# Optimization experiments

Measured on AMD Instinct MI355X. Metric: run time of the kernel, lower is better.

## Reference

```python
import jax, jax.numpy as jnp
import numpy as np

N_IN, N_HID, N_OUT = 128, 256, 128
B, T = 64, 2048


def setup_inputs() -> dict:
    key = jax.random.key(0)
    ks = jax.random.split(key, 10)
    s_in = 1.0 / np.sqrt(N_IN)
    s_h = 1.0 / np.sqrt(N_HID)
    return {
        "input_signal": jax.random.normal(ks[0], (B, T, N_IN), dtype=jnp.float32),
        "W_in": jax.random.uniform(ks[1], (N_HID, N_IN), jnp.float32, -s_in, s_in),
        "b_in": jax.random.uniform(ks[2], (N_HID,), jnp.float32, -s_in, s_in),
        "W_ih": jax.random.uniform(ks[3], (N_HID, N_HID), jnp.float32, -s_h, s_h),
        "b_ih": jax.random.uniform(ks[4], (N_HID,), jnp.float32, -s_h, s_h),
        "W_hh": jax.random.uniform(ks[5], (N_HID, N_HID), jnp.float32, -s_h, s_h),
        "b_hh": jax.random.uniform(ks[6], (N_HID,), jnp.float32, -s_h, s_h),
        "W_out": jax.random.uniform(ks[7], (N_OUT, N_HID), jnp.float32, -s_h, s_h),
        "b_out": jax.random.uniform(ks[8], (N_OUT,), jnp.float32, -s_h, s_h),
    }


def reference(input_signal, W_in, b_in, W_ih, b_ih, W_hh, b_hh, W_out, b_out):
    # x_t = relu(in_layer(u_t)); h_t = relu(tanh(W_ih x_t + b_ih + W_hh h_{t-1} + b_hh))
    # out_t = out_layer(h_t)
    x = jax.nn.relu(jnp.einsum('bti,hi->bth', input_signal, W_in) + b_in)
    # Precompute the input-to-hidden projection for all timesteps (batched GEMM),
    # leaving only the sequential h @ W_hh recurrence inside the scan.
    pre = jnp.einsum('bth,gh->tbg', x, W_ih) + b_ih  # [T, B, H]
    h0 = jnp.zeros((input_signal.shape[0], W_hh.shape[0]), dtype=input_signal.dtype)

    def step(h, pre_t):
        h_new = jax.nn.relu(jnp.tanh(pre_t + h @ W_hh.T + b_hh))
        return h_new, h_new

    _, hs = jax.lax.scan(step, h0, pre)            # hs: [T, B, H]
    hidden_list = jnp.transpose(hs, (1, 0, 2))     # [B, T, H]
    output_list = jnp.einsum('bth,oh->bto', hidden_list, W_out) + b_out  # [B, T, O]
    return hidden_list, output_list
```

## Files before the change

kernel.cpp:

```cpp
#include <hip/hip_runtime.h>
#include <hip/hip_fp16.h>

typedef _Float16 f16;
typedef __attribute__((ext_vector_type(2))) _Float16 f16x2;
typedef __attribute__((ext_vector_type(8))) _Float16 f16x8;
typedef __attribute__((ext_vector_type(4))) float f32x4;

constexpr int BATCH = 64;
constexpr int TLEN  = 2048;
constexpr int NIN   = 128;
constexpr int NHID  = 256;
constexpr int NOUT  = 128;
constexpr long MROWS = (long)BATCH * TLEN;
constexpr float CSC = 2.8853900817779268f;

__device__ __forceinline__ float exp2f_hw(float x) {
#if __has_builtin(__builtin_amdgcn_exp2f)
  return __builtin_amdgcn_exp2f(x);
#else
  return __expf(x * 0.6931471805599453f);
#endif
}
__device__ __forceinline__ float rcp_hw(float x) {
#if __has_builtin(__builtin_amdgcn_rcpf)
  return __builtin_amdgcn_rcpf(x);
#else
  return 1.0f / x;
#endif
}
__device__ __forceinline__ float fdot2f(unsigned int a, unsigned int b, float c) {
#if __has_builtin(__builtin_amdgcn_fdot2)
  return __builtin_amdgcn_fdot2(__builtin_bit_cast(f16x2, a),
                                __builtin_bit_cast(f16x2, b), c, false);
#else
  f16x2 av = __builtin_bit_cast(f16x2, a);
  f16x2 bv = __builtin_bit_cast(f16x2, b);
  return c + (float)av.x * (float)bv.x + (float)av.y * (float)bv.y;
#endif
}
template<int CTRL>
__device__ __forceinline__ float dpp_xor(float x) {
  int r = __builtin_amdgcn_update_dpp(0, __builtin_bit_cast(int, x),
                                      CTRL, 0xF, 0xF, true);
  return __builtin_bit_cast(float, r);
}
__device__ __forceinline__ void barrier_lds() {
  asm volatile("s_waitcnt lgkmcnt(0)" ::: "memory");
  __builtin_amdgcn_s_barrier();
  asm volatile("" ::: "memory");
}

__global__ void cvt_weights(const float* __restrict__ Win, const float* __restrict__ Wih,
                            const float* __restrict__ Whh, const float* __restrict__ Wout,
                            f16* __restrict__ dst) {
  int i = blockIdx.x * blockDim.x + threadIdx.x;
  if (i < 32768) {
    float v = Win[i]; f16 h = (f16)v;
    dst[i] = h; dst[32768 + i] = (f16)(v - (float)h);
  } else if (i < 98304) {
    int j = i - 32768; float v = Wih[j]; f16 h = (f16)v;
    dst[65536 + j] = h; dst[131072 + j] = (f16)(v - (float)h);
  } else if (i < 163840) {
    int j = i - 98304; dst[196608 + j] = (f16)(CSC * Whh[j]);
  } else if (i < 196608) {
    int j = i - 163840; dst[262144 + j] = (f16)Wout[j];
  }
}

constexpr int BM = 64, BN = 64, BK = 64;

template<int MODE>
__global__ __launch_bounds__(256)
void gemm_kernel(const void* __restrict__ Ap, const void* __restrict__ Ap2,
                 const f16* __restrict__ Bh_, const f16* __restrict__ Bl_,
                 const float* __restrict__ bias, const float* __restrict__ bias2,
                 void* __restrict__ Cp, void* __restrict__ Cp2,
                 int K, int N) {
  __shared__ __align__(16) f16 Ah[BM][BK + 8];
  __shared__ __align__(16) f16 Al[BM][BK + 8];
  __shared__ __align__(16) f16 Bh[BN][BK + 8];
  __shared__ __align__(16) f16 Bl[BN][BK + 8];

  const int tid  = threadIdx.x;
  const int lane = tid & 63;
  const int wid  = tid >> 6;
  const int wm = wid >> 1, wn = wid & 1;
  const long row0 = (long)blockIdx.x * BM;
  const int  col0 = blockIdx.y * BN;
  const int r  = tid >> 2;
  const int cc = (tid & 3) * 16;

  f32x4 acc[2][2] = {};

  for (int k0 = 0; k0 < K; k0 += BK) {
    if constexpr (MODE == 1) {
      const float* src = (const float*)Ap + (row0 + r) * (long)K + k0 + cc;
      #pragma unroll
      for (int q = 0; q < 4; ++q) {
        float4 v = ((const float4*)src)[q];
        f16 h0 = (f16)v.x, h1 = (f16)v.y, h2 = (f16)v.z, h3 = (f16)v.w;
        Ah[r][cc + 4*q + 0] = h0;  Al[r][cc + 4*q + 0] = (f16)(v.x - (float)h0);
        Ah[r][cc + 4*q + 1] = h1;  Al[r][cc + 4*q + 1] = (f16)(v.y - (float)h1);
        Ah[r][cc + 4*q + 2] = h2;  Al[r][cc + 4*q + 2] = (f16)(v.z - (float)h2);
        Ah[r][cc + 4*q + 3] = h3;  Al[r][cc + 4*q + 3] = (f16)(v.w - (float)h3);
      }
    } else if constexpr (MODE == 2) {
      const f16* sh = (const f16*)Ap  + (row0 + r) * (long)K + k0 + cc;
      const f16* sl = (const f16*)Ap2 + (row0 + r) * (long)K + k0 + cc;
      *(uint4*)&Ah[r][cc]     = *(const uint4*)sh;
      *(uint4*)&Ah[r][cc + 8] = *(const uint4*)(sh + 8);
      *(uint4*)&Al[r][cc]     = *(const uint4*)sl;
      *(uint4*)&Al[r][cc + 8] = *(const uint4*)(sl + 8);
    } else {
      const f16* sh = (const f16*)Ap + (row0 + r) * (long)K + k0 + cc;
      *(uint4*)&Ah[r][cc]     = *(const uint4*)sh;
      *(uint4*)&Ah[r][cc + 8] = *(const uint4*)(sh + 8);
    }
    {
      const f16* sh = Bh_ + (col0 + r) * (long)K + k0 + cc;
      *(uint4*)&Bh[r][cc]     = *(const uint4*)sh;
      *(uint4*)&Bh[r][cc + 8] = *(const uint4*)(sh + 8);
      if constexpr (MODE != 3) {
        const f16* sl = Bl_ + (col0 + r) * (long)K + k0 + cc;
        *(uint4*)&Bl[r][cc]     = *(const uint4*)sl;
        *(uint4*)&Bl[r][cc + 8] = *(const uint4*)(sl + 8);
      }
    }
    __syncthreads();

    #pragma unroll
    for (int ks = 0; ks < BK / 32; ++ks) {
      const int ko = ks * 32 + (lane >> 4) * 8;
      const int ra = wm * 32 + (lane & 15);
      const int rb = wn * 32 + (lane & 15);
      f16x8 a0 = *(const f16x8*)&Ah[ra][ko];
      f16x8 a1 = *(const f16x8*)&Ah[ra + 16][ko];
      f16x8 b0 = *(const f16x8*)&Bh[rb][ko];
      f16x8 b1 = *(const f16x8*)&Bh[rb + 16][ko];
      acc[0][0] = __builtin_amdgcn_mfma_f32_16x16x32_f16(a0, b0, acc[0][0], 0, 0, 0);
      acc[0][1] = __builtin_amdgcn_mfma_f32_16x16x32_f16(a0, b1, acc[0][1], 0, 0, 0);
      acc[1][0] = __builtin_amdgcn_mfma_f32_16x16x32_f16(a1, b0, acc[1][0], 0, 0, 0);
      acc[1][1] = __builtin_amdgcn_mfma_f32_16x16x32_f16(a1, b1, acc[1][1], 0, 0, 0);
      if constexpr (MODE != 3) {
        f16x8 la0 = *(const f16x8*)&Al[ra][ko];
        f16x8 la1 = *(const f16x8*)&Al[ra + 16][ko];
        f16x8 lb0 = *(const f16x8*)&Bl[rb][ko];
        f16x8 lb1 = *(const f16x8*)&Bl[rb + 16][ko];
        acc[0][0] = __builtin_amdgcn_mfma_f32_16x16x32_f16(a0, lb0, acc[0][0], 0, 0, 0);
        acc[0][0] = __builtin_amdgcn_mfma_f32_16x16x32_f16(la0, b0, acc[0][0], 0, 0, 0);
        acc[0][1] = __builtin_amdgcn_mfma_f32_16x16x32_f16(a0, lb1, acc[0][1], 0, 0, 0);
        acc[0][1] = __builtin_amdgcn_mfma_f32_16x16x32_f16(la0, b1, acc[0][1], 0, 0, 0);
        acc[1][0] = __builtin_amdgcn_mfma_f32_16x16x32_f16(a1, lb0, acc[1][0], 0, 0, 0);
        acc[1][0] = __builtin_amdgcn_mfma_f32_16x16x32_f16(la1, b0, acc[1][0], 0, 0, 0);
        acc[1][1] = __builtin_amdgcn_mfma_f32_16x16x32_f16(a1, lb1, acc[1][1], 0, 0, 0);
        acc[1][1] = __builtin_amdgcn_mfma_f32_16x16x32_f16(la1, b1, acc[1][1], 0, 0, 0);
      }
    }
    __syncthreads();
  }

  #pragma unroll
  for (int mi = 0; mi < 2; ++mi)
    #pragma unroll
    for (int ni = 0; ni < 2; ++ni)
      #pragma unroll
      for (int q = 0; q < 4; ++q) {
        long row = row0 + wm * 32 + mi * 16 + (lane >> 4) * 4 + q;
        int  col = col0 + wn * 32 + ni * 16 + (lane & 15);
        if constexpr (MODE == 1) {
          float v = fmaxf(acc[mi][ni][q] + bias[col], 0.0f);
          f16 h = (f16)v;
          ((f16*)Cp )[row * (long)N + col] = h;
          ((f16*)Cp2)[row * (long)N + col] = (f16)(v - (float)h);
        } else if constexpr (MODE == 2) {
          float v = (acc[mi][ni][q] + bias[col] + bias2[col]) * CSC;
          ((float*)Cp)[row * (long)N + col] = v;
        } else {
          ((float*)Cp)[row * (long)N + col] = acc[mi][ni][q] + bias[col];
        }
      }
}

#define STEP(K, SRC, DST, P) do {                                            \
  unsigned int hs[32];                                                       \
  _Pragma("unroll")                                                          \
  for (int q = 0; q < 8; ++q) {                                              \
    uint4 v = *(const uint4*)((SRC) + roff[q]);                              \
    hs[4*q+0] = v.x; hs[4*q+1] = v.y; hs[4*q+2] = v.z; hs[4*q+3] = v.w;      \
  }                                                                          \
  float a0a = 0.f, a1a = 0.f, a0b = 0.f, a1b = 0.f;                          \
  _Pragma("unroll")                                                          \
  for (int kk = 0; kk < 16; ++kk) {                                          \
    a0a = fdot2f(wr0[kk], hs[kk], a0a);                                      \
    a1a = fdot2f(wr1[kk], hs[kk], a1a);                                      \
  }                                                                          \
  _Pragma("unroll")                                                          \
  for (int kk = 16; kk < 32; ++kk) {                                         \
    a0b = fdot2f(wr0[kk], hs[kk], a0b);                                      \
    a1b = fdot2f(wr1[kk], hs[kk], a1b);                                      \
  }                                                                          \
  float a0 = a0a + a0b, a1 = a1a + a1b;                                      \
  float keep = s0 ? a1 : a0;                                                 \
  float send = s0 ? a0 : a1;                                                 \
  float t1 = keep + dpp_xor<0xB1>(send);       \
  float z  = t1 + dpp_xor<0x4E>(t1) + (P);              \
  float ee = exp2f_hw(z);                                                    \
  float hv = fmaxf(fmaf(-2.0f, rcp_hw(ee + 1.0f), 1.0f), 0.0f);              \
  f16 hf = (f16)hv;                                                          \
  if (!s1) *(f16*)((DST) + wo) = hf;              \
  else     hp[(K) * 256] = hf;                  \
} while (0)

__global__ __launch_bounds__(512, 1)
void rec_kernel(const float* __restrict__ pre, const f16* __restrict__ W2,
                f16* __restrict__ h16) {
  const int b    = blockIdx.x;
  const int tid  = threadIdx.x;
  const int lane = tid & 63;
  const int w    = tid >> 6;
  const int jj   = lane & 3;
  const int grp  = (lane >> 2) | (w << 4);
  const int s0   = lane & 1;
  const int s1   = (lane >> 1) & 1;
  const int G    = grp * 2;
  const int g    = G + s0;

  __shared__ __align__(16) char hb[2][512];

  unsigned int wr0[32], wr1[32];
  #pragma unroll
  for (int q = 0; q < 8; ++q) {
    int c = (q + 2 * jj) & 7;
    uint4 v0 = *(const uint4*)(W2 + (size_t)G * 256 + 64 * jj + 8 * c);
    uint4 v1 = *(const uint4*)(W2 + (size_t)(G + 1) * 256 + 64 * jj + 8 * c);
    wr0[4*q+0] = v0.x; wr0[4*q+1] = v0.y; wr0[4*q+2] = v0.z; wr0[4*q+3] = v0.w;
    wr1[4*q+0] = v1.x; wr1[4*q+1] = v1.y; wr1[4*q+2] = v1.z; wr1[4*q+3] = v1.w;
  }
  if (tid < 128) ((unsigned int*)&hb[0][0])[tid] = 0u;
  __syncthreads();

  int roff[8];
  #pragma unroll
  for (int q = 0; q < 8; ++q) roff[q] = 128 * jj + 16 * ((q + 2 * jj) & 7);
  const int wo = 2 * g;

  const float* pp  = pre + (size_t)b * TLEN * 256 + g;
  f16*         hp  = h16 + (size_t)b * TLEN * 256 + g;
  const float* ppf = pp + 1024;

  float p0 = pp[0];
  float p1 = pp[256];
  float p2 = pp[512];
  float p3 = pp[768];

  const char* hb0 = &hb[0][0];
  char*       hb1 = &hb[1][0];

  #pragma unroll 1
  for (int t = 0; t < TLEN; t += 4) {
    float n0 = ppf[0];
    float n1 = ppf[256];
    float n2 = ppf[512];
    float n3 = ppf[768];
    STEP(0, hb0, hb1, p0);
    barrier_lds();
    STEP(1, hb1, (char*)hb0, p1);
    barrier_lds();
    STEP(2, hb0, hb1, p2);
    barrier_lds();
    STEP(3, hb1, (char*)hb0, p3);
    barrier_lds();
    p0 = n0; p1 = n1; p2 = n2; p3 = n3;
    ppf += 1024;
    hp  += 1024;
  }
}

__global__ __launch_bounds__(256)
void cvt_h(const f16* __restrict__ src, float* __restrict__ dst, long n) {
  long i0 = ((long)blockIdx.x * 256 + threadIdx.x) * 8;
  long stride = (long)gridDim.x * 256 * 8;
  for (long i = i0; i < n; i += stride) {
    f16x8 v = *(const f16x8*)(src + i);
    float4 a = {(float)v[0], (float)v[1], (float)v[2], (float)v[3]};
    float4 bq = {(float)v[4], (float)v[5], (float)v[6], (float)v[7]};
    *(float4*)(dst + i) = a;
    *(float4*)(dst + i + 4) = bq;
  }
}

extern "C" void kernel_launch(void* const* d_in, const int* in_sizes, int n_in,
                              void* d_out, int out_size, void* d_ws, size_t ws_size,
                              hipStream_t stream) {
  const float* input = (const float*)d_in[0];
  const float* W_in  = (const float*)d_in[1];
  const float* b_in  = (const float*)d_in[2];
  const float* W_ih  = (const float*)d_in[3];
  const float* b_ih  = (const float*)d_in[4];
  const float* W_hh  = (const float*)d_in[5];
  const float* b_hh  = (const float*)d_in[6];
  const float* W_out = (const float*)d_in[7];
  const float* b_out = (const float*)d_in[8];

  float* hidden = (float*)d_out;
  float* outp   = (float*)d_out + MROWS * NHID;

  char* ws = (char*)d_ws;
  const size_t xh_off  = 0;
  const size_t xl_off  = (size_t)MROWS * NHID * 2;
  const size_t pre_off = xl_off * 2;
  const size_t w_off   = pre_off + (size_t)MROWS * NHID * 4;
  const size_t need    = w_off + 294912ull * 2;
  if (ws_size < need) return;

  f16*   x_hi  = (f16*)(ws + xh_off);
  f16*   x_lo  = (f16*)(ws + xl_off);
  float* pre   = (float*)(ws + pre_off);
  f16*   wbase = (f16*)(ws + w_off);
  f16 *WinH = wbase,           *WinL = wbase + 32768;
  f16 *WihH = wbase + 65536,   *WihL = wbase + 131072;
  f16 *Whh16 = wbase + 196608, *Wout16 = wbase + 262144;
  f16* h16 = x_hi;

  cvt_weights<<<768, 256, 0, stream>>>(W_in, W_ih, W_hh, W_out, wbase);

  dim3 g12((unsigned)(MROWS / BM), NHID / BN);
  gemm_kernel<1><<<g12, 256, 0, stream>>>(input, nullptr, WinH, WinL, b_in, nullptr,
                                          x_hi, x_lo, NIN, NHID);
  gemm_kernel<2><<<g12, 256, 0, stream>>>(x_hi, x_lo, WihH, WihL, b_ih, b_hh,
                                          pre, nullptr, NHID, NHID);

  rec_kernel<<<BATCH, 512, 0, stream>>>(pre, Whh16, h16);

  cvt_h<<<2048, 256, 0, stream>>>(h16, hidden, MROWS * NHID);

  dim3 g3((unsigned)(MROWS / BM), NOUT / BN);
  gemm_kernel<3><<<g3, 256, 0, stream>>>(h16, nullptr, Wout16, nullptr, b_out, nullptr,
                                         outp, nullptr, NHID, NOUT);
}
```

Before: 1.108 ms.

## Run recurrence on MFMA with eight batches per block in time-major layout

The recurrent step moves from per-lane fdot2 dot products, one block per batch, to MFMA 16x16x32 f16 tiles. Each block now handles 8 batch rows (half of the 16 MFMA columns), so the launch shrinks from 64 blocks to 8. The pre-activation GEMM now writes its output time-major so each step's loads are contiguous across batches, and the hidden state goes through swizzled LDS double buffers. The aim is to cut per-step latency of the serial chain with matrix cores, at the cost of using far fewer CUs and leaving half of each MFMA idle.

```diff
diff --git a/kernel.cpp b/kernel.cpp
--- a/kernel.cpp
+++ b/kernel.cpp
@@ -3,6 +3,7 @@
 
 typedef _Float16 f16;
 typedef __attribute__((ext_vector_type(2))) _Float16 f16x2;
+typedef __attribute__((ext_vector_type(4))) _Float16 f16x4;
 typedef __attribute__((ext_vector_type(8))) _Float16 f16x8;
 typedef __attribute__((ext_vector_type(4))) float f32x4;
 
@@ -27,22 +28,6 @@
 #else
   return 1.0f / x;
 #endif
-}
-__device__ __forceinline__ float fdot2f(unsigned int a, unsigned int b, float c) {
-#if __has_builtin(__builtin_amdgcn_fdot2)
-  return __builtin_amdgcn_fdot2(__builtin_bit_cast(f16x2, a),
-                                __builtin_bit_cast(f16x2, b), c, false);
-#else
-  f16x2 av = __builtin_bit_cast(f16x2, a);
-  f16x2 bv = __builtin_bit_cast(f16x2, b);
-  return c + (float)av.x * (float)bv.x + (float)av.y * (float)bv.y;
-#endif
-}
-template<int CTRL>
-__device__ __forceinline__ float dpp_xor(float x) {
-  int r = __builtin_amdgcn_update_dpp(0, __builtin_bit_cast(int, x),
-                                      CTRL, 0xF, 0xF, true);
-  return __builtin_bit_cast(float, r);
 }
 __device__ __forceinline__ void barrier_lds() {
   asm volatile("s_waitcnt lgkmcnt(0)" ::: "memory");
@@ -174,104 +159,125 @@
           ((f16*)Cp2)[row * (long)N + col] = (f16)(v - (float)h);
         } else if constexpr (MODE == 2) {
           float v = (acc[mi][ni][q] + bias[col] + bias2[col]) * CSC;
-          ((float*)Cp)[row * (long)N + col] = v;
+          long prow = (row & (long)(TLEN - 1)) * BATCH + (row >> 11);
+          ((float*)Cp)[prow * (long)N + col] = v;
         } else {
           ((float*)Cp)[row * (long)N + col] = acc[mi][ni][q] + bias[col];
         }
       }
 }
 
-#define STEP(K, SRC, DST, P) do {                                            \
-  unsigned int hs[32];                                                       \
-  _Pragma("unroll")                                                          \
-  for (int q = 0; q < 8; ++q) {                                              \
-    uint4 v = *(const uint4*)((SRC) + roff[q]);                              \
-    hs[4*q+0] = v.x; hs[4*q+1] = v.y; hs[4*q+2] = v.z; hs[4*q+3] = v.w;      \
-  }                                                                          \
-  float a0a = 0.f, a1a = 0.f, a0b = 0.f, a1b = 0.f;                          \
-  _Pragma("unroll")                                                          \
-  for (int kk = 0; kk < 16; ++kk) {                                          \
-    a0a = fdot2f(wr0[kk], hs[kk], a0a);                                      \
-    a1a = fdot2f(wr1[kk], hs[kk], a1a);                                      \
-  }                                                                          \
-  _Pragma("unroll")                                                          \
-  for (int kk = 16; kk < 32; ++kk) {                                         \
-    a0b = fdot2f(wr0[kk], hs[kk], a0b);                                      \
-    a1b = fdot2f(wr1[kk], hs[kk], a1b);                                      \
-  }                                                                          \
-  float a0 = a0a + a0b, a1 = a1a + a1b;                                      \
-  float keep = s0 ? a1 : a0;                                                 \
-  float send = s0 ? a0 : a1;                                                 \
-  float t1 = keep + dpp_xor<0xB1>(send);       \
-  float z  = t1 + dpp_xor<0x4E>(t1) + (P);              \
-  float ee = exp2f_hw(z);                                                    \
-  float hv = fmaxf(fmaf(-2.0f, rcp_hw(ee + 1.0f), 1.0f), 0.0f);              \
-  f16 hf = (f16)hv;                                                          \
-  if (!s1) *(f16*)((DST) + wo) = hf;              \
-  else     hp[(K) * 256] = hf;                  \
+#define RSTEP(S, SO, DO_, P0, P1) do {                                        \
+  if (valid) {                                                                \
+    _Pragma("unroll")                                                         \
+    for (int c = 0; c < 8; ++c)                                               \
+      hB[c] = *(const f16x8*)(hbase + (SO) + roff[c]);                        \
+  }                                                                           \
+  f32x4 aA0 = (P0), aA1 = (P1);                                               \
+  f32x4 aB0 = {0.f, 0.f, 0.f, 0.f};                                           \
+  f32x4 aB1 = {0.f, 0.f, 0.f, 0.f};                                           \
+  _Pragma("unroll")                                                           \
+  for (int c = 0; c < 4; ++c) {                                               \
+    aA0 = __builtin_amdgcn_mfma_f32_16x16x32_f16(wA[0][c],     hB[c],     aA0, 0, 0, 0); \
+    aA1 = __builtin_amdgcn_mfma_f32_16x16x32_f16(wA[1][c],     hB[c],     aA1, 0, 0, 0); \
+    aB0 = __builtin_amdgcn_mfma_f32_16x16x32_f16(wA[0][c + 4], hB[c + 4], aB0, 0, 0, 0); \
+    aB1 = __builtin_amdgcn_mfma_f32_16x16x32_f16(wA[1][c + 4], hB[c + 4], aB1, 0, 0, 0); \
+  }                                                                           \
+  f16x4 h0, h1;                                                               \
+  _Pragma("unroll")                                                           \
+  for (int q = 0; q < 4; ++q) {                                               \
+    float z0 = aA0[q] + aB0[q];                                               \
+    float z1 = aA1[q] + aB1[q];                                               \
+    float e0 = exp2f_hw(z0);                                                  \
+    float e1 = exp2f_hw(z1);                                                  \
+    float v0 = fmaxf(fmaf(-2.0f, rcp_hw(e0 + 1.0f), 1.0f), 0.0f);             \
+    float v1 = fmaxf(fmaf(-2.0f, rcp_hw(e1 + 1.0f), 1.0f), 0.0f);             \
+    h0[q] = (f16)v0;                                                          \
+    h1[q] = (f16)v1;                                                          \
+  }                                                                           \
+  if (valid) {                                                                \
+    *(f16x4*)(hbase + (DO_) + wb0) = h0;              \
+    *(f16x4*)(hbase + (DO_) + wb1) = h1;              \
+    *(f16x4*)(hp + (S) * 256)      = h0;              \
+    *(f16x4*)(hp + (S) * 256 + 16) = h1;              \
+  }                                                                           \
+  barrier_lds();                                                              \
 } while (0)
 
 __global__ __launch_bounds__(512, 1)
-void rec_kernel(const float* __restrict__ pre, const f16* __restrict__ W2,
-                f16* __restrict__ h16) {
-  const int b    = blockIdx.x;
+void rec_mfma(const float* __restrict__ pre, const f16* __restrict__ Whh,
+              f16* __restrict__ h16) {
+  const int blk  = blockIdx.x;
   const int tid  = threadIdx.x;
   const int lane = tid & 63;
   const int w    = tid >> 6;
-  const int jj   = lane & 3;
-  const int grp  = (lane >> 2) | (w << 4);
-  const int s0   = lane & 1;
-  const int s1   = (lane >> 1) & 1;
-  const int G    = grp * 2;
-  const int g    = G + s0;
-
-  __shared__ __align__(16) char hb[2][512];
-
-  unsigned int wr0[32], wr1[32];
+  const int col  = lane & 15;
+  const int kg   = lane >> 4;
+  const bool valid = (col < 8);
+  const int bq   = col & 7;
+  const long bglob = (long)blk * 8 + bq;
+
+  __shared__ __align__(16) char hb[8192];
+  char* hbase = (char*)hb;
+
+  f16x8 wA[2][8];
   #pragma unroll
-  for (int q = 0; q < 8; ++q) {
-    int c = (q + 2 * jj) & 7;
-    uint4 v0 = *(const uint4*)(W2 + (size_t)G * 256 + 64 * jj + 8 * c);
-    uint4 v1 = *(const uint4*)(W2 + (size_t)(G + 1) * 256 + 64 * jj + 8 * c);
-    wr0[4*q+0] = v0.x; wr0[4*q+1] = v0.y; wr0[4*q+2] = v0.z; wr0[4*q+3] = v0.w;
-    wr1[4*q+0] = v1.x; wr1[4*q+1] = v1.y; wr1[4*q+2] = v1.z; wr1[4*q+3] = v1.w;
-  }
-  if (tid < 128) ((unsigned int*)&hb[0][0])[tid] = 0u;
+  for (int t = 0; t < 2; ++t)
+    #pragma unroll
+    for (int c = 0; c < 8; ++c)
+      wA[t][c] = *(const f16x8*)(Whh + (size_t)(32 * w + 16 * t + col) * 256
+                                 + c * 32 + kg * 8);
+
+  {
+    uint4 z = {0u, 0u, 0u, 0u};
+    *(uint4*)(hbase + tid * 16) = z;
+  }
   __syncthreads();
 
+  const int rbase = bq * 512 + ((kg * 16) ^ ((bq & 3) << 4)) + ((bq & 4) << 4);
   int roff[8];
   #pragma unroll
-  for (int q = 0; q < 8; ++q) roff[q] = 128 * jj + 16 * ((q + 2 * jj) & 7);
-  const int wo = 2 * g;
-
-  const float* pp  = pre + (size_t)b * TLEN * 256 + g;
-  f16*         hp  = h16 + (size_t)b * TLEN * 256 + g;
-  const float* ppf = pp + 1024;
-
-  float p0 = pp[0];
-  float p1 = pp[256];
-  float p2 = pp[512];
-  float p3 = pp[768];
-
-  const char* hb0 = &hb[0][0];
-  char*       hb1 = &hb[1][0];
+  for (int c = 0; c < 8; ++c) roff[c] = rbase ^ (c * 64);
+  const int wb0   = bq * 512 + ((8 * kg) ^ ((bq & 1) << 4)) + ((bq & 2) << 4)
+                  + ((64 * w) ^ ((bq & 4) << 4));
+  const int wb1   = wb0 ^ 32;
+
+  const float* pp  = pre + (size_t)bglob * 256 + 32 * w + 4 * kg;
+  f16*         hp  = h16 + (size_t)bglob * TLEN * 256 + 32 * w + 4 * kg;
+  const float* ppf = pp + 4 * 16384;
+
+  f32x4 p00 = *(const f32x4*)(pp);
+  f32x4 p01 = *(const f32x4*)(pp + 16);
+  f32x4 p10 = *(const f32x4*)(pp + 16384);
+  f32x4 p11 = *(const f32x4*)(pp + 16400);
+  f32x4 p20 = *(const f32x4*)(pp + 32768);
+  f32x4 p21 = *(const f32x4*)(pp + 32784);
+  f32x4 p30 = *(const f32x4*)(pp + 49152);
+  f32x4 p31 = *(const f32x4*)(pp + 49168);
+
+  f16x8 hB[8] = {};
 
   #pragma unroll 1
   for (int t = 0; t < TLEN; t += 4) {
-    float n0 = ppf[0];
-    float n1 = ppf[256];
-    float n2 = ppf[512];
-    float n3 = ppf[768];
-    STEP(0, hb0, hb1, p0);
-    barrier_lds();
-    STEP(1, hb1, (char*)hb0, p1);
-    barrier_lds();
-    STEP(2, hb0, hb1, p2);
-    barrier_lds();
-    STEP(3, hb1, (char*)hb0, p3);
-    barrier_lds();
-    p0 = n0; p1 = n1; p2 = n2; p3 = n3;
-    ppf += 1024;
+    f32x4 n00 = {}, n01 = {}, n10 = {}, n11 = {};
+    f32x4 n20 = {}, n21 = {}, n30 = {}, n31 = {};
+    if (t + 4 < TLEN) {
+      n00 = *(const f32x4*)(ppf);
+      n01 = *(const f32x4*)(ppf + 16);
+      n10 = *(const f32x4*)(ppf + 16384);
+      n11 = *(const f32x4*)(ppf + 16400);
+      n20 = *(const f32x4*)(ppf + 32768);
+      n21 = *(const f32x4*)(ppf + 32784);
+      n30 = *(const f32x4*)(ppf + 49152);
+      n31 = *(const f32x4*)(ppf + 49168);
+    }
+    RSTEP(0, 0,    4096, p00, p01);
+    RSTEP(1, 4096, 0,    p10, p11);
+    RSTEP(2, 0,    4096, p20, p21);
+    RSTEP(3, 4096, 0,    p30, p31);
+    p00 = n00; p01 = n01; p10 = n10; p11 = n11;
+    p20 = n20; p21 = n21; p30 = n30; p31 = n31;
+    ppf += 65536;
     hp  += 1024;
   }
 }
@@ -330,7 +336,7 @@
   gemm_kernel<2><<<g12, 256, 0, stream>>>(x_hi, x_lo, WihH, WihL, b_ih, b_hh,
                                           pre, nullptr, NHID, NHID);
 
-  rec_kernel<<<BATCH, 512, 0, stream>>>(pre, Whh16, h16);
+  rec_mfma<<<8, 512, 0, stream>>>(pre, Whh16, h16);
 
   cvt_h<<<2048, 256, 0, stream>>>(h16, hidden, MROWS * NHID);
 
```

Measured after the change: 1.984 ms. +79.0%, slower.

## Split recurrence K-dimension eight ways per output group with cross-half permlane reduction

Applied to the files above, without the earlier changes.

Changes the recurrent matvec work split so each lane covers a 32-wide K slice for 4 hidden outputs (eight lanes per group of four), instead of a 64-wide slice for 2 outputs. Each step now does half as many LDS reads and dot products per lane, at the cost of an extra reduction stage that swaps values between wave halves with permlane32_swap or ds_bpermute. The aim is a shorter per-step critical path in the sequential recurrence. The extra cross-lane hop adds latency, and the LDS and W_hh access patterns are remapped.

```diff
diff --git a/kernel.cpp b/kernel.cpp
--- a/kernel.cpp
+++ b/kernel.cpp
@@ -43,6 +43,18 @@
   int r = __builtin_amdgcn_update_dpp(0, __builtin_bit_cast(int, x),
                                       CTRL, 0xF, 0xF, true);
   return __builtin_bit_cast(float, r);
+}
+__device__ __forceinline__ float xor32_partner(float x, int lane) {
+#if __has_builtin(__builtin_amdgcn_permlane32_swap)
+  auto r = __builtin_amdgcn_permlane32_swap(
+      __builtin_bit_cast(unsigned int, x), __builtin_bit_cast(unsigned int, x),
+      false, false);
+  unsigned int pv = (lane < 32) ? r[1] : r[0];
+  return __builtin_bit_cast(float, pv);
+#else
+  return __builtin_bit_cast(float, __builtin_amdgcn_ds_bpermute(
+      ((lane ^ 32) << 2), __builtin_bit_cast(int, x)));
+#endif
 }
 __device__ __forceinline__ void barrier_lds() {
   asm volatile("s_waitcnt lgkmcnt(0)" ::: "memory");
@@ -182,33 +194,45 @@
 }
 
 #define STEP(K, SRC, DST, P) do {                                            \
-  unsigned int hs[32];                                                       \
+  unsigned int hs[16];                                                       \
   _Pragma("unroll")                                                          \
-  for (int q = 0; q < 8; ++q) {                                              \
+  for (int q = 0; q < 4; ++q) {                                              \
     uint4 v = *(const uint4*)((SRC) + roff[q]);                              \
     hs[4*q+0] = v.x; hs[4*q+1] = v.y; hs[4*q+2] = v.z; hs[4*q+3] = v.w;      \
   }                                                                          \
-  float a0a = 0.f, a1a = 0.f, a0b = 0.f, a1b = 0.f;                          \
+  float sA0 = 0.f, sA1 = 0.f, sA2 = 0.f, sA3 = 0.f;                          \
+  float sB0 = 0.f, sB1 = 0.f, sB2 = 0.f, sB3 = 0.f;                          \
   _Pragma("unroll")                                                          \
-  for (int kk = 0; kk < 16; ++kk) {                                          \
-    a0a = fdot2f(wr0[kk], hs[kk], a0a);                                      \
-    a1a = fdot2f(wr1[kk], hs[kk], a1a);                                      \
+  for (int m = 0; m < 8; ++m) {                                              \
+    sA0 = fdot2f(wr[0][m], hs[m], sA0);                                      \
+    sA1 = fdot2f(wr[1][m], hs[m], sA1);                                      \
+    sA2 = fdot2f(wr[2][m], hs[m], sA2);                                      \
+    sA3 = fdot2f(wr[3][m], hs[m], sA3);                                      \
   }                                                                          \
   _Pragma("unroll")                                                          \
-  for (int kk = 16; kk < 32; ++kk) {                                         \
-    a0b = fdot2f(wr0[kk], hs[kk], a0b);                                      \
-    a1b = fdot2f(wr1[kk], hs[kk], a1b);                                      \
+  for (int m = 8; m < 16; ++m) {                                             \
+    sB0 = fdot2f(wr[0][m], hs[m], sB0);                                      \
+    sB1 = fdot2f(wr[1][m], hs[m], sB1);                                      \
+    sB2 = fdot2f(wr[2][m], hs[m], sB2);                                      \
+    sB3 = fdot2f(wr[3][m], hs[m], sB3);                                      \
   }                                                                          \
-  float a0 = a0a + a0b, a1 = a1a + a1b;                                      \
-  float keep = s0 ? a1 : a0;                                                 \
-  float send = s0 ? a0 : a1;                                                 \
-  float t1 = keep + dpp_xor<0xB1>(send);       \
-  float z  = t1 + dpp_xor<0x4E>(t1) + (P);              \
+  float sv0 = sA0 + sB0, sv1 = sA1 + sB1;                                    \
+  float sv2 = sA2 + sB2, sv3 = sA3 + sB3;                                    \
+                               \
+  float k0 = s0 ? sv1 : sv0, d0 = s0 ? sv0 : sv1;                            \
+  float k1 = s0 ? sv3 : sv2, d1 = s0 ? sv2 : sv3;                            \
+  float t0 = k0 + dpp_xor<0xB1>(d0);                                         \
+  float t1 = k1 + dpp_xor<0xB1>(d1);                                         \
+                              \
+  float rk = s1 ? t1 : t0, rs = s1 ? t0 : t1;                                \
+  float z2 = rk + dpp_xor<0x4E>(rs);                                         \
+                                                \
+  float z  = z2 + xor32_partner(z2, lane) + (P);                             \
   float ee = exp2f_hw(z);                                                    \
   float hv = fmaxf(fmaf(-2.0f, rcp_hw(ee + 1.0f), 1.0f), 0.0f);              \
   f16 hf = (f16)hv;                                                          \
-  if (!s1) *(f16*)((DST) + wo) = hf;              \
-  else     hp[(K) * 256] = hf;                  \
+  if (lane < 32) *(f16*)((DST) + wo) = hf;        \
+  else           hp[(K) * 256] = hf;            \
 } while (0)
 
 __global__ __launch_bounds__(512, 1)
@@ -218,30 +242,29 @@
   const int tid  = threadIdx.x;
   const int lane = tid & 63;
   const int w    = tid >> 6;
-  const int jj   = lane & 3;
-  const int grp  = (lane >> 2) | (w << 4);
+  const int jj   = (lane & 3) | ((lane >> 5) << 2);
   const int s0   = lane & 1;
   const int s1   = (lane >> 1) & 1;
-  const int G    = grp * 2;
-  const int g    = G + s0;
+  const int G8   = ((lane >> 2) & 7) | (w << 3);
+  const int g    = 32 * w + (lane & 31);
 
   __shared__ __align__(16) char hb[2][512];
 
-  unsigned int wr0[32], wr1[32];
+  unsigned int wr[4][16];
   #pragma unroll
-  for (int q = 0; q < 8; ++q) {
-    int c = (q + 2 * jj) & 7;
-    uint4 v0 = *(const uint4*)(W2 + (size_t)G * 256 + 64 * jj + 8 * c);
-    uint4 v1 = *(const uint4*)(W2 + (size_t)(G + 1) * 256 + 64 * jj + 8 * c);
-    wr0[4*q+0] = v0.x; wr0[4*q+1] = v0.y; wr0[4*q+2] = v0.z; wr0[4*q+3] = v0.w;
-    wr1[4*q+0] = v1.x; wr1[4*q+1] = v1.y; wr1[4*q+2] = v1.z; wr1[4*q+3] = v1.w;
-  }
+  for (int i = 0; i < 4; ++i)
+    #pragma unroll
+    for (int q = 0; q < 4; ++q) {
+      int c = (q + jj) & 3;
+      uint4 v = *(const uint4*)(W2 + (size_t)(4 * G8 + i) * 256 + 32 * jj + 8 * c);
+      wr[i][4*q+0] = v.x; wr[i][4*q+1] = v.y; wr[i][4*q+2] = v.z; wr[i][4*q+3] = v.w;
+    }
   if (tid < 128) ((unsigned int*)&hb[0][0])[tid] = 0u;
   __syncthreads();
 
-  int roff[8];
+  int roff[4];
   #pragma unroll
-  for (int q = 0; q < 8; ++q) roff[q] = 128 * jj + 16 * ((q + 2 * jj) & 7);
+  for (int q = 0; q < 4; ++q) roff[q] = 64 * jj + 16 * ((q + jj) & 3);
   const int wo = 2 * g;
 
   const float* pp  = pre + (size_t)b * TLEN * 256 + g;
```

After: 1.194 ms. 7.8% more time.

## Use MFMA 16x16x32 f16 for the recurrent matvec instead of dot2 plus DPP

Applied to the files above, without the earlier changes.

Replaces the per-lane fdot2 dot products and DPP cross-lane reductions in the sequential recurrence with MFMA 16x16x32 f16 instructions. Each wave holds 32 rows of W_hh as MFMA A-operands and broadcasts the hidden state as the B operand. Only one column of the output tile is actually used. Pre-activations are loaded as f32x4 vectors and h is written in f16x4 chunks. This trades wasted MFMA throughput (15 of 16 columns unused) for fewer instructions and no shuffle reductions on the latency-critical per-step path, but MFMA latency may dominate each step.

```diff
diff --git a/kernel.cpp b/kernel.cpp
--- a/kernel.cpp
+++ b/kernel.cpp
@@ -3,6 +3,7 @@
 
 typedef _Float16 f16;
 typedef __attribute__((ext_vector_type(2))) _Float16 f16x2;
+typedef __attribute__((ext_vector_type(4))) _Float16 f16x4;
 typedef __attribute__((ext_vector_type(8))) _Float16 f16x8;
 typedef __attribute__((ext_vector_type(4))) float f32x4;
 
@@ -27,22 +28,6 @@
 #else
   return 1.0f / x;
 #endif
-}
-__device__ __forceinline__ float fdot2f(unsigned int a, unsigned int b, float c) {
-#if __has_builtin(__builtin_amdgcn_fdot2)
-  return __builtin_amdgcn_fdot2(__builtin_bit_cast(f16x2, a),
-                                __builtin_bit_cast(f16x2, b), c, false);
-#else
-  f16x2 av = __builtin_bit_cast(f16x2, a);
-  f16x2 bv = __builtin_bit_cast(f16x2, b);
-  return c + (float)av.x * (float)bv.x + (float)av.y * (float)bv.y;
-#endif
-}
-template<int CTRL>
-__device__ __forceinline__ float dpp_xor(float x) {
-  int r = __builtin_amdgcn_update_dpp(0, __builtin_bit_cast(int, x),
-                                      CTRL, 0xF, 0xF, true);
-  return __builtin_bit_cast(float, r);
 }
 __device__ __forceinline__ void barrier_lds() {
   asm volatile("s_waitcnt lgkmcnt(0)" ::: "memory");
@@ -181,34 +166,39 @@
       }
 }
 
-#define STEP(K, SRC, DST, P) do {                                            \
-  unsigned int hs[32];                                                       \
+#define RSTEP(S, SRC, DST, PA, PB) do {                                      \
+  f16x8 hB[8];                                                               \
   _Pragma("unroll")                                                          \
-  for (int q = 0; q < 8; ++q) {                                              \
-    uint4 v = *(const uint4*)((SRC) + roff[q]);                              \
-    hs[4*q+0] = v.x; hs[4*q+1] = v.y; hs[4*q+2] = v.z; hs[4*q+3] = v.w;      \
+  for (int c = 0; c < 8; ++c)                                                \
+    hB[c] = *(const f16x8*)((SRC) + 64 * c + 16 * kg);                       \
+  f32x4 aA0 = {0.f,0.f,0.f,0.f}, aB0 = {0.f,0.f,0.f,0.f};                    \
+  f32x4 aA1 = {0.f,0.f,0.f,0.f}, aB1 = {0.f,0.f,0.f,0.f};                    \
+  _Pragma("unroll")                                                          \
+  for (int c = 0; c < 4; ++c) {                                              \
+    aA0 = __builtin_amdgcn_mfma_f32_16x16x32_f16(wA[0][c],     hB[c],     aA0, 0, 0, 0); \
+    aA1 = __builtin_amdgcn_mfma_f32_16x16x32_f16(wA[1][c],     hB[c],     aA1, 0, 0, 0); \
+    aB0 = __builtin_amdgcn_mfma_f32_16x16x32_f16(wA[0][c + 4], hB[c + 4], aB0, 0, 0, 0); \
+    aB1 = __builtin_amdgcn_mfma_f32_16x16x32_f16(wA[1][c + 4], hB[c + 4], aB1, 0, 0, 0); \
   }                                                                          \
-  float a0a = 0.f, a1a = 0.f, a0b = 0.f, a1b = 0.f;                          \
+  f16x4 h0, h1;                                                              \
   _Pragma("unroll")                                                          \
-  for (int kk = 0; kk < 16; ++kk) {                                          \
-    a0a = fdot2f(wr0[kk], hs[kk], a0a);                                      \
-    a1a = fdot2f(wr1[kk], hs[kk], a1a);                                      \
+  for (int q = 0; q < 4; ++q) {                                              \
+    float z0 = aA0[q] + aB0[q] + (PA)[q];                                    \
+    float z1 = aA1[q] + aB1[q] + (PB)[q];                                    \
+    float e0 = exp2f_hw(z0);                                                 \
+    float e1 = exp2f_hw(z1);                                                 \
+    float v0 = fmaxf(fmaf(-2.0f, rcp_hw(e0 + 1.0f), 1.0f), 0.0f);            \
+    float v1 = fmaxf(fmaf(-2.0f, rcp_hw(e1 + 1.0f), 1.0f), 0.0f);            \
+    h0[q] = (f16)v0;                                                         \
+    h1[q] = (f16)v1;                                                         \
   }                                                                          \
-  _Pragma("unroll")                                                          \
-  for (int kk = 16; kk < 32; ++kk) {                                         \
-    a0b = fdot2f(wr0[kk], hs[kk], a0b);                                      \
-    a1b = fdot2f(wr1[kk], hs[kk], a1b);                                      \
+  if (col == 0) {                                                            \
+    *(f16x4*)((DST) + wo)      = h0;         \
+    *(f16x4*)((DST) + wo + 32) = h1;         \
+  } else if (col == 1) {                                                     \
+    *(f16x4*)(hp + (S) * 256)      = h0;              \
+    *(f16x4*)(hp + (S) * 256 + 16) = h1;              \
   }                                                                          \
-  float a0 = a0a + a0b, a1 = a1a + a1b;                                      \
-  float keep = s0 ? a1 : a0;                                                 \
-  float send = s0 ? a0 : a1;                                                 \
-  float t1 = keep + dpp_xor<0xB1>(send);       \
-  float z  = t1 + dpp_xor<0x4E>(t1) + (P);              \
-  float ee = exp2f_hw(z);                                                    \
-  float hv = fmaxf(fmaf(-2.0f, rcp_hw(ee + 1.0f), 1.0f), 0.0f);              \
-  f16 hf = (f16)hv;                                                          \
-  if (!s1) *(f16*)((DST) + wo) = hf;              \
-  else     hp[(K) * 256] = hf;                  \
 } while (0)
 
 __global__ __launch_bounds__(512, 1)
@@ -218,59 +208,61 @@
   const int tid  = threadIdx.x;
   const int lane = tid & 63;
   const int w    = tid >> 6;
-  const int jj   = lane & 3;
-  const int grp  = (lane >> 2) | (w << 4);
-  const int s0   = lane & 1;
-  const int s1   = (lane >> 1) & 1;
-  const int G    = grp * 2;
-  const int g    = G + s0;
+  const int col  = lane & 15;
+  const int kg   = lane >> 4;
 
   __shared__ __align__(16) char hb[2][512];
 
-  unsigned int wr0[32], wr1[32];
+  f16x8 wA[2][8];
   #pragma unroll
-  for (int q = 0; q < 8; ++q) {
-    int c = (q + 2 * jj) & 7;
-    uint4 v0 = *(const uint4*)(W2 + (size_t)G * 256 + 64 * jj + 8 * c);
-    uint4 v1 = *(const uint4*)(W2 + (size_t)(G + 1) * 256 + 64 * jj + 8 * c);
-    wr0[4*q+0] = v0.x; wr0[4*q+1] = v0.y; wr0[4*q+2] = v0.z; wr0[4*q+3] = v0.w;
-    wr1[4*q+0] = v1.x; wr1[4*q+1] = v1.y; wr1[4*q+2] = v1.z; wr1[4*q+3] = v1.w;
-  }
-  if (tid < 128) ((unsigned int*)&hb[0][0])[tid] = 0u;
+  for (int t = 0; t < 2; ++t)
+    #pragma unroll
+    for (int c = 0; c < 8; ++c)
+      wA[t][c] = *(const f16x8*)(W2 + (size_t)(32 * w + 16 * t + col) * 256
+                                 + c * 32 + kg * 8);
+
+  if (tid < 256) ((unsigned int*)&hb[0][0])[tid] = 0u;
   __syncthreads();
 
-  int roff[8];
-  #pragma unroll
-  for (int q = 0; q < 8; ++q) roff[q] = 128 * jj + 16 * ((q + 2 * jj) & 7);
-  const int wo = 2 * g;
-
-  const float* pp  = pre + (size_t)b * TLEN * 256 + g;
-  f16*         hp  = h16 + (size_t)b * TLEN * 256 + g;
+  const int wo = 64 * w + 8 * kg;
+  const int g0 = 32 * w + 4 * kg;
+
+  const float* pp  = pre + (size_t)b * TLEN * 256 + g0;
+  f16*         hp  = h16 + (size_t)b * TLEN * 256 + g0;
   const float* ppf = pp + 1024;
 
-  float p0 = pp[0];
-  float p1 = pp[256];
-  float p2 = pp[512];
-  float p3 = pp[768];
+  f32x4 p00 = *(const f32x4*)(pp);
+  f32x4 p01 = *(const f32x4*)(pp + 16);
+  f32x4 p10 = *(const f32x4*)(pp + 256);
+  f32x4 p11 = *(const f32x4*)(pp + 272);
+  f32x4 p20 = *(const f32x4*)(pp + 512);
+  f32x4 p21 = *(const f32x4*)(pp + 528);
+  f32x4 p30 = *(const f32x4*)(pp + 768);
+  f32x4 p31 = *(const f32x4*)(pp + 784);
 
   const char* hb0 = &hb[0][0];
   char*       hb1 = &hb[1][0];
 
   #pragma unroll 1
   for (int t = 0; t < TLEN; t += 4) {
-    float n0 = ppf[0];
-    float n1 = ppf[256];
-    float n2 = ppf[512];
-    float n3 = ppf[768];
-    STEP(0, hb0, hb1, p0);
+    f32x4 n00 = *(const f32x4*)(ppf);
+    f32x4 n01 = *(const f32x4*)(ppf + 16);
+    f32x4 n10 = *(const f32x4*)(ppf + 256);
+    f32x4 n11 = *(const f32x4*)(ppf + 272);
+    f32x4 n20 = *(const f32x4*)(ppf + 512);
+    f32x4 n21 = *(const f32x4*)(ppf + 528);
+    f32x4 n30 = *(const f32x4*)(ppf + 768);
+    f32x4 n31 = *(const f32x4*)(ppf + 784);
+    RSTEP(0, hb0, hb1, p00, p01);
     barrier_lds();
-    STEP(1, hb1, (char*)hb0, p1);
+    RSTEP(1, hb1, (char*)hb0, p10, p11);
     barrier_lds();
-    STEP(2, hb0, hb1, p2);
+    RSTEP(2, hb0, hb1, p20, p21);
     barrier_lds();
-    STEP(3, hb1, (char*)hb0, p3);
+    RSTEP(3, hb1, (char*)hb0, p30, p31);
     barrier_lds();
-    p0 = n0; p1 = n1; p2 = n2; p3 = n3;
+    p00 = n00; p01 = n01; p10 = n10; p11 = n11;
+    p20 = n20; p21 = n21; p30 = n30; p31 = n31;
     ppf += 1024;
     hp  += 1024;
   }
```

Result: slower. 1.529 ms (+38.0%).
